# Kernel optimization log

Hardware: AMD Instinct MI355X
Metric: run time of the kernel (lower is better)

## Reference

```python
import jax, jax.numpy as jnp
import numpy as np

B, S, D = 2, 2048, 7168
R, H, VD = 1024, 16, 128
QK_HD = R // H            # 64, per-head latent q/k dim
SCALE = float(np.sqrt(D // H))  # self.scale = d_heads ** 0.5 = sqrt(448)


def setup_inputs() -> dict:
    key = jax.random.key(0)
    ks = jax.random.split(key, 6)
    return {
        "x":   jax.random.normal(ks[0], (B, S, D), dtype=jnp.float32),
        "Wq":  jax.random.normal(ks[1], (R, D), dtype=jnp.float32) * 0.02,
        "Wkv": jax.random.normal(ks[2], (R, D), dtype=jnp.float32) * 0.02,
        "Wvb": jax.random.normal(ks[3], (H * VD, R), dtype=jnp.float32) * 0.02,
        "Wo":  jax.random.normal(ks[4], (D, H * VD), dtype=jnp.float32) * 0.02,
        "bo":  jnp.zeros((D,), dtype=jnp.float32),
    }


def reference(x, Wq, Wkv, Wvb, Wo, bo):
    b, s, d = x.shape
    # low-rank compressed projections (torch Linear: y = x @ W.T)
    q_lat  = x @ Wq.T            # [B,S,R] compressed query
    kv_lat = x @ Wkv.T           # [B,S,R] compressed KV latent (shared K)
    q = q_lat.reshape(b, s, H, QK_HD)    # [B,S,H,64]
    k = kv_lat.reshape(b, s, H, QK_HD)   # [B,S,H,64]
    # up-project values from latent
    v = (kv_lat @ Wvb.T).reshape(b, s, H, VD)  # [B,S,H,128]
    # scaled causal attention in latent head space
    scores = jnp.einsum("bqhd,bkhd->bhqk", q, k) / SCALE  # [B,H,S,S]
    causal = jnp.tril(jnp.ones((s, s), dtype=bool))
    scores = jnp.where(causal, scores, jnp.finfo(scores.dtype).min)
    attn = jax.nn.softmax(scores, axis=-1)
    out = jnp.einsum("bhqk,bkhd->bqhd", attn, v).reshape(b, s, H * VD)
    return out @ Wo.T + bo       # [B,S,D]
```

## Files before the change

### kernel.cpp

```cpp
#include <hip/hip_runtime.h>
#include <hip/hip_bf16.h>

typedef __bf16 bf16_t;
typedef __attribute__((ext_vector_type(8))) __bf16 bf16x8;
typedef __attribute__((ext_vector_type(4))) __bf16 bf16x4;
typedef __attribute__((ext_vector_type(4))) float f32x4;

#define B_ 2
#define S_ 2048
#define D_ 7168
#define R_ 1024
#define H_ 16
#define VD_ 128
#define MROWS 4096
#define NQKV 2048
#define HVD 2048

__device__ __forceinline__ void gload_lds16(const bf16_t* g, bf16_t* l) {
    __builtin_amdgcn_global_load_lds(
        (const __attribute__((address_space(1))) unsigned int*)(g),
        (__attribute__((address_space(3))) unsigned int*)(l),
        16, 0, 0);
}

__global__ __launch_bounds__(256)
void cvt_f32_bf16(const float* __restrict__ src, bf16_t* __restrict__ dst, float scale) {
    size_t i = ((size_t)blockIdx.x * 256 + threadIdx.x) * 4;
    f32x4 v = *(const f32x4*)(src + i);
    bf16x4 o;
    o[0] = (bf16_t)(v[0] * scale);
    o[1] = (bf16_t)(v[1] * scale);
    o[2] = (bf16_t)(v[2] * scale);
    o[3] = (bf16_t)(v[3] * scale);
    *(bf16x4*)(dst + i) = o;
}

template<int OUTF32>
__global__ __launch_bounds__(256)
void gemm_bt(const bf16_t* __restrict__ A, int lda,
             const bf16_t* __restrict__ Bt, int ldb,
             void* __restrict__ Cv, int ldc,
             const float* __restrict__ bias, int K)
{
    __shared__ __align__(16) bf16_t As[2][128 * 64];
    __shared__ __align__(16) bf16_t Bs[2][128 * 64];
    const int tid  = threadIdx.x;
    const int lane = tid & 63;
    const int wave = tid >> 6;
    const int tileM = blockIdx.y * 128;
    const int tileN = blockIdx.x * 128;
    const int wr = (wave >> 1) * 64;
    const int wc = (wave & 1) * 64;
    const int r  = lane & 15;
    const int kq = lane >> 4;

    const bf16_t* Ag = A  + (size_t)tileM * lda;
    const bf16_t* Bg = Bt + (size_t)tileN * ldb;

    int srow[4], scol[4], slin[4];
    #pragma unroll
    for (int i = 0; i < 4; ++i) {
        slin[i] = (i * 256 + tid) * 8;
        srow[i] = slin[i] >> 6;
        scol[i] = (slin[i] & 63) ^ ((srow[i] & 7) << 3);
    }

    #define ISSUE_TILE(buf, k0)                                                  \
        {                                                                        \
            _Pragma("unroll")                                                    \
            for (int i = 0; i < 4; ++i) {                                        \
                gload_lds16(Ag + (size_t)srow[i] * lda + (k0) + scol[i], As[buf] + slin[i]); \
                gload_lds16(Bg + (size_t)srow[i] * ldb + (k0) + scol[i], Bs[buf] + slin[i]); \
            }                                                                    \
        }

    f32x4 acc[4][4] = {};
    const int nt = K >> 6;

    ISSUE_TILE(0, 0)
    ISSUE_TILE(1, 64)
    asm volatile("s_waitcnt vmcnt(8)" ::: "memory");
    __builtin_amdgcn_s_barrier();
    __builtin_amdgcn_sched_barrier(0);

    for (int t = 0; t < nt; ++t) {
        const int cur = t & 1;
        const bf16_t* Ab = As[cur];
        const bf16_t* Bb = Bs[cur];

        bf16x8 af[4][2], bfr[4][2];
        #pragma unroll
        for (int m = 0; m < 4; ++m)
            #pragma unroll
            for (int kk = 0; kk < 2; ++kk) {
                const int e = (wr + m * 16 + r) * 64 + kk * 32 + kq * 8;
                af[m][kk] = *(const bf16x8*)(Ab + (e ^ ((r & 7) << 3)));
            }
        #pragma unroll
        for (int n = 0; n < 4; ++n)
            #pragma unroll
            for (int kk = 0; kk < 2; ++kk) {
                const int e = (wc + n * 16 + r) * 64 + kk * 32 + kq * 8;
                bfr[n][kk] = *(const bf16x8*)(Bb + (e ^ ((r & 7) << 3)));
            }
        __builtin_amdgcn_s_setprio(1);
        #pragma unroll
        for (int kk = 0; kk < 2; ++kk)
            #pragma unroll
            for (int m = 0; m < 4; ++m)
                #pragma unroll
                for (int n = 0; n < 4; ++n)
                    acc[m][n] = __builtin_amdgcn_mfma_f32_16x16x32_bf16(af[m][kk], bfr[n][kk], acc[m][n], 0, 0, 0);
        __builtin_amdgcn_s_setprio(0);

        __builtin_amdgcn_s_barrier();
        __builtin_amdgcn_sched_barrier(0);
        if (t + 2 < nt) {
            ISSUE_TILE(cur, (t + 2) << 6)
            asm volatile("s_waitcnt vmcnt(8)" ::: "memory");
        } else {
            asm volatile("s_waitcnt vmcnt(0)" ::: "memory");
        }
        __builtin_amdgcn_s_barrier();
        __builtin_amdgcn_sched_barrier(0);
    }
    #undef ISSUE_TILE

    const int orow = tileM + wr + kq * 4;
    const int ocol = tileN + wc + r;
    if (OUTF32) {
        float* C = (float*)Cv;
        #pragma unroll
        for (int n = 0; n < 4; ++n) {
            float bv = bias[ocol + n * 16];
            #pragma unroll
            for (int m = 0; m < 4; ++m)
                #pragma unroll
                for (int j = 0; j < 4; ++j)
                    C[(size_t)(orow + m * 16 + j) * ldc + ocol + n * 16] = acc[m][n][j] + bv;
        }
    } else {
        bf16_t* C = (bf16_t*)Cv;
        #pragma unroll
        for (int m = 0; m < 4; ++m)
            #pragma unroll
            for (int n = 0; n < 4; ++n)
                #pragma unroll
                for (int j = 0; j < 4; ++j)
                    C[(size_t)(orow + m * 16 + j) * ldc + ocol + n * 16] = (bf16_t)acc[m][n][j];
    }
}

template<int OUTF32>
__global__ __launch_bounds__(512, 2)
void gemm_bt256(const bf16_t* __restrict__ A, int lda,
                const bf16_t* __restrict__ Bt, int ldb,
                void* __restrict__ Cv, int ldc,
                const float* __restrict__ bias, int K)
{
    __shared__ __align__(16) bf16_t As[2][256 * 64];
    __shared__ __align__(16) bf16_t Bs[2][256 * 64];
    const int tid  = threadIdx.x;
    const int lane = tid & 63;
    const int wave = tid >> 6;
    const int wm = wave >> 2;
    const int wn = wave & 3;
    const int tileM = blockIdx.y * 256;
    const int tileN = blockIdx.x * 256;
    const int r  = lane & 15;
    const int kq = lane >> 4;

    const bf16_t* Ag = A  + (size_t)tileM * lda;
    const bf16_t* Bg = Bt + (size_t)tileN * ldb;

    int srow[4], scol[4], slin[4];
    #pragma unroll
    for (int i = 0; i < 4; ++i) {
        slin[i] = (i * 512 + tid) * 8;
        srow[i] = slin[i] >> 6;
        scol[i] = (slin[i] & 63) ^ ((srow[i] & 7) << 3);
    }

    #define ISSUE_TILE2(buf, k0)                                                 \
        {                                                                        \
            _Pragma("unroll")                                                    \
            for (int i = 0; i < 4; ++i) {                                        \
                gload_lds16(Ag + (size_t)srow[i] * lda + (k0) + scol[i], As[buf] + slin[i]); \
                gload_lds16(Bg + (size_t)srow[i] * ldb + (k0) + scol[i], Bs[buf] + slin[i]); \
            }                                                                    \
        }

    f32x4 acc[8][4] = {};
    const int nt = K >> 6;

    ISSUE_TILE2(0, 0)
    ISSUE_TILE2(1, 64)
    asm volatile("s_waitcnt vmcnt(8)" ::: "memory");
    __builtin_amdgcn_s_barrier();
    __builtin_amdgcn_sched_barrier(0);

    for (int t = 0; t < nt; ++t) {
        const int cur = t & 1;
        const bf16_t* Ab = As[cur];
        const bf16_t* Bb = Bs[cur];

        #pragma unroll
        for (int kk = 0; kk < 2; ++kk) {
            bf16x8 af[8], bfr[4];
            #pragma unroll
            for (int m = 0; m < 8; ++m) {
                const int e = (wm * 128 + m * 16 + r) * 64 + kk * 32 + kq * 8;
                af[m] = *(const bf16x8*)(Ab + (e ^ ((r & 7) << 3)));
            }
            #pragma unroll
            for (int n = 0; n < 4; ++n) {
                const int e = (wn * 64 + n * 16 + r) * 64 + kk * 32 + kq * 8;
                bfr[n] = *(const bf16x8*)(Bb + (e ^ ((r & 7) << 3)));
            }
            __builtin_amdgcn_s_setprio(1);
            #pragma unroll
            for (int m = 0; m < 8; ++m)
                #pragma unroll
                for (int n = 0; n < 4; ++n)
                    acc[m][n] = __builtin_amdgcn_mfma_f32_16x16x32_bf16(af[m], bfr[n], acc[m][n], 0, 0, 0);
            __builtin_amdgcn_s_setprio(0);
        }

        __builtin_amdgcn_s_barrier();
        __builtin_amdgcn_sched_barrier(0);
        if (t + 2 < nt) {
            ISSUE_TILE2(cur, (t + 2) << 6)
            asm volatile("s_waitcnt vmcnt(8)" ::: "memory");
        } else {
            asm volatile("s_waitcnt vmcnt(0)" ::: "memory");
        }
        __builtin_amdgcn_s_barrier();
        __builtin_amdgcn_sched_barrier(0);
    }
    #undef ISSUE_TILE2

    const int orow = tileM + wm * 128 + kq * 4;
    const int ocol = tileN + wn * 64 + r;
    if (OUTF32) {
        float* C = (float*)Cv;
        #pragma unroll
        for (int n = 0; n < 4; ++n) {
            float bv = bias[ocol + n * 16];
            #pragma unroll
            for (int m = 0; m < 8; ++m)
                #pragma unroll
                for (int j = 0; j < 4; ++j)
                    C[(size_t)(orow + m * 16 + j) * ldc + ocol + n * 16] = acc[m][n][j] + bv;
        }
    } else {
        bf16_t* C = (bf16_t*)Cv;
        #pragma unroll
        for (int m = 0; m < 8; ++m)
            #pragma unroll
            for (int n = 0; n < 4; ++n)
                #pragma unroll
                for (int j = 0; j < 4; ++j)
                    C[(size_t)(orow + m * 16 + j) * ldc + ocol + n * 16] = (bf16_t)acc[m][n][j];
    }
}

__device__ __forceinline__ void attn_qtile(
    const bf16_t* __restrict__ Q, const bf16_t* __restrict__ Kp,
    const bf16_t* __restrict__ Vp, bf16_t* __restrict__ Op,
    bf16_t* __restrict__ P_lds, int qbase, int lane)
{
    const int r  = lane & 15;
    const int kq = lane >> 4;

    bf16x8 qf[2][2];
    #pragma unroll
    for (int m = 0; m < 2; ++m)
        #pragma unroll
        for (int kk = 0; kk < 2; ++kk)
            qf[m][kk] = *(const bf16x8*)(Q + (size_t)(qbase + m * 16 + r) * NQKV + kk * 32 + kq * 8);

    f32x4 o[2][8] = {};
    float mst[2][4], lst[2][4];
    #pragma unroll
    for (int m = 0; m < 2; ++m)
        #pragma unroll
        for (int j = 0; j < 4; ++j) { mst[m][j] = -INFINITY; lst[m][j] = 0.0f; }

    const int nfull  = qbase >> 6;
    const int ntiles = (qbase + 95) >> 6;

    for (int t = 0; t < ntiles; ++t) {
        const int kvb = t * 64;
        f32x4 s[2][4] = {};
        #pragma unroll
        for (int n = 0; n < 4; ++n) {
            bf16x8 kf0 = *(const bf16x8*)(Kp + (size_t)(kvb + n * 16 + r) * NQKV + kq * 8);
            bf16x8 kf1 = *(const bf16x8*)(Kp + (size_t)(kvb + n * 16 + r) * NQKV + 32 + kq * 8);
            #pragma unroll
            for (int m = 0; m < 2; ++m) {
                s[m][n] = __builtin_amdgcn_mfma_f32_16x16x32_bf16(qf[m][0], kf0, s[m][n], 0, 0, 0);
                s[m][n] = __builtin_amdgcn_mfma_f32_16x16x32_bf16(qf[m][1], kf1, s[m][n], 0, 0, 0);
            }
        }
        if (t >= nfull) {
            #pragma unroll
            for (int m = 0; m < 2; ++m)
                #pragma unroll
                for (int n = 0; n < 4; ++n)
                    #pragma unroll
                    for (int j = 0; j < 4; ++j) {
                        int kc = kvb + n * 16 + r;
                        int qr = qbase + m * 16 + kq * 4 + j;
                        if (kc > qr) s[m][n][j] = -1e30f;
                    }
        }
        float mx[2][4];
        #pragma unroll
        for (int m = 0; m < 2; ++m)
            #pragma unroll
            for (int j = 0; j < 4; ++j) {
                float v = fmaxf(fmaxf(s[m][0][j], s[m][1][j]), fmaxf(s[m][2][j], s[m][3][j]));
                #pragma unroll
                for (int d = 1; d < 16; d <<= 1) v = fmaxf(v, __shfl_xor(v, d, 64));
                mx[m][j] = v;
            }
        bool need = false;
        #pragma unroll
        for (int m = 0; m < 2; ++m)
            #pragma unroll
            for (int j = 0; j < 4; ++j) need |= (mx[m][j] > mst[m][j] + 8.0f);
        if (__ballot(need)) {
            #pragma unroll
            for (int m = 0; m < 2; ++m)
                #pragma unroll
                for (int j = 0; j < 4; ++j) {
                    float mnew  = fmaxf(mst[m][j], mx[m][j]);
                    float alpha = __expf(mst[m][j] - mnew);
                    lst[m][j] *= alpha;
                    mst[m][j]  = mnew;
                    #pragma unroll
                    for (int n = 0; n < 8; ++n) o[m][n][j] *= alpha;
                }
        }
        #pragma unroll
        for (int m = 0; m < 2; ++m)
            #pragma unroll
            for (int j = 0; j < 4; ++j) {
                float rs = 0.0f;
                const int row = m * 16 + kq * 4 + j;
                #pragma unroll
                for (int n = 0; n < 4; ++n) {
                    float pv = __expf(s[m][n][j] - mst[m][j]);
                    rs += pv;
                    const int c = (n * 16 + r) ^ ((row & 7) << 3);
                    P_lds[row * 64 + c] = (bf16_t)pv;
                }
                #pragma unroll
                for (int d = 1; d < 16; d <<= 1) rs += __shfl_xor(rs, d, 64);
                lst[m][j] += rs;
            }
        __syncthreads();
        bf16x8 pf[2][2];
        #pragma unroll
        for (int m = 0; m < 2; ++m)
            #pragma unroll
            for (int kk = 0; kk < 2; ++kk) {
                const int e = (m * 16 + r) * 64 + kk * 32 + kq * 8;
                pf[m][kk] = *(const bf16x8*)(P_lds + (e ^ ((r & 7) << 3)));
            }
        #pragma unroll
        for (int n = 0; n < 8; ++n) {
            #pragma unroll
            for (int kk = 0; kk < 2; ++kk) {
                bf16x8 vf = *(const bf16x8*)(Vp + (size_t)(n * 16 + r) * MROWS + kvb + kk * 32 + kq * 8);
                #pragma unroll
                for (int m = 0; m < 2; ++m)
                    o[m][n] = __builtin_amdgcn_mfma_f32_16x16x32_bf16(pf[m][kk], vf, o[m][n], 0, 0, 0);
            }
        }
        __syncthreads();
    }

    #pragma unroll
    for (int m = 0; m < 2; ++m)
        #pragma unroll
        for (int j = 0; j < 4; ++j) {
            float inv = 1.0f / lst[m][j];
            int row = m * 16 + kq * 4 + j;
            #pragma unroll
            for (int n = 0; n < 8; ++n)
                Op[(size_t)(qbase + row) * HVD + n * 16 + r] = (bf16_t)(o[m][n][j] * inv);
        }
}

__global__ __launch_bounds__(64)
void attn_kernel(const bf16_t* __restrict__ qkv, const bf16_t* __restrict__ Vt,
                 bf16_t* __restrict__ O)
{
    __shared__ __align__(16) bf16_t P_lds[32 * 64];
    const int lane = threadIdx.x;
    const int p = blockIdx.x;
    const int h = blockIdx.y;
    const int b = blockIdx.z;

    const bf16_t* Q  = qkv + (size_t)(b * S_) * NQKV + h * 64;
    const bf16_t* Kp = qkv + (size_t)(b * S_) * NQKV + R_ + h * 64;
    const bf16_t* Vp = Vt + (size_t)(h * VD_) * MROWS + b * S_;
    bf16_t* Op = O + (size_t)(b * S_) * HVD + h * VD_;

    attn_qtile(Q, Kp, Vp, Op, P_lds, (63 - p) * 32, lane);
    attn_qtile(Q, Kp, Vp, Op, P_lds, p * 32, lane);
}

extern "C" void kernel_launch(void* const* d_in, const int* in_sizes, int n_in,
                              void* d_out, int out_size, void* d_ws, size_t ws_size,
                              hipStream_t stream) {
    const float* x   = (const float*)d_in[0];
    const float* Wq  = (const float*)d_in[1];
    const float* Wkv = (const float*)d_in[2];
    const float* Wvb = (const float*)d_in[3];
    const float* Wo  = (const float*)d_in[4];
    const float* bo  = (const float*)d_in[5];

    char* oc = (char*)d_out;
    bf16_t* xb     = (bf16_t*)oc;
    bf16_t* Wqkv_b = (bf16_t*)(oc + 58720256);
    char* ws = (char*)d_ws;
    bf16_t* qkv_b  = (bf16_t*)ws;
    bf16_t* Wvb_b  = (bf16_t*)(ws + 16777216);
    bf16_t* Vt_b   = (bf16_t*)(ws + 20971520);
    bf16_t* attn_b = (bf16_t*)(ws + 37748736);
    bf16_t* Wo_b   = (bf16_t*)(ws + 54525952);

    const float inv_scale = 0.047245559f;

    cvt_f32_bf16<<<29360128 / 1024, 256, 0, stream>>>(x,   xb, 1.0f);
    cvt_f32_bf16<<< 7340032 / 1024, 256, 0, stream>>>(Wq,  Wqkv_b, inv_scale);
    cvt_f32_bf16<<< 7340032 / 1024, 256, 0, stream>>>(Wkv, Wqkv_b + 7340032, 1.0f);
    cvt_f32_bf16<<< 2097152 / 1024, 256, 0, stream>>>(Wvb, Wvb_b, 1.0f);
    cvt_f32_bf16<<<14680064 / 1024, 256, 0, stream>>>(Wo,  Wo_b, 1.0f);

    gemm_bt<0><<<dim3(16, 32), 256, 0, stream>>>(xb, D_, Wqkv_b, D_, qkv_b, NQKV, nullptr, D_);
    gemm_bt<0><<<dim3(32, 16), 256, 0, stream>>>(Wvb_b, R_, qkv_b + R_, NQKV, Vt_b, MROWS, nullptr, R_);
    attn_kernel<<<dim3(32, H_, B_), 64, 0, stream>>>(qkv_b, Vt_b, attn_b);
    gemm_bt256<1><<<dim3(28, 16), 512, 0, stream>>>(attn_b, HVD, Wo_b, HVD, d_out, D_, bo, HVD);
}
```

Before: 518.0 us.

## Overlap next-tile global loads with second k-half MFMAs and split attention across waves

Both GEMM kernels now split each 64-wide k tile into two halves. The second half's fragments are read from LDS early, then a barrier is hit and the global-to-LDS prefetch for tile t+2 is issued before the second-half MFMAs, so the loads overlap compute instead of sitting between barriers. The attention kernel now runs its two causal q-tiles on two waves of one 128-thread block, each with its own P buffer, rather than one wave doing both in sequence. The __syncthreads calls inside the attention loop are removed, which relies on each wave only touching its own LDS slice.

```diff
diff --git a/kernel.cpp b/kernel.cpp
--- a/kernel.cpp
+++ b/kernel.cpp
@@ -88,39 +88,53 @@
         const bf16_t* Ab = As[cur];
         const bf16_t* Bb = Bs[cur];
 
-        bf16x8 af[4][2], bfr[4][2];
+        bf16x8 af0[4], bf0[4];
+        #pragma unroll
+        for (int m = 0; m < 4; ++m) {
+            const int e = (wr + m * 16 + r) * 64 + kq * 8;
+            af0[m] = *(const bf16x8*)(Ab + (e ^ ((r & 7) << 3)));
+        }
+        #pragma unroll
+        for (int n = 0; n < 4; ++n) {
+            const int e = (wc + n * 16 + r) * 64 + kq * 8;
+            bf0[n] = *(const bf16x8*)(Bb + (e ^ ((r & 7) << 3)));
+        }
+        __builtin_amdgcn_s_setprio(1);
         #pragma unroll
         for (int m = 0; m < 4; ++m)
             #pragma unroll
-            for (int kk = 0; kk < 2; ++kk) {
-                const int e = (wr + m * 16 + r) * 64 + kk * 32 + kq * 8;
-                af[m][kk] = *(const bf16x8*)(Ab + (e ^ ((r & 7) << 3)));
-            }
-        #pragma unroll
-        for (int n = 0; n < 4; ++n)
-            #pragma unroll
-            for (int kk = 0; kk < 2; ++kk) {
-                const int e = (wc + n * 16 + r) * 64 + kk * 32 + kq * 8;
-                bfr[n][kk] = *(const bf16x8*)(Bb + (e ^ ((r & 7) << 3)));
-            }
+            for (int n = 0; n < 4; ++n)
+                acc[m][n] = __builtin_amdgcn_mfma_f32_16x16x32_bf16(af0[m], bf0[n], acc[m][n], 0, 0, 0);
+        __builtin_amdgcn_s_setprio(0);
+
+        bf16x8 af1[4], bf1[4];
+        #pragma unroll
+        for (int m = 0; m < 4; ++m) {
+            const int e = (wr + m * 16 + r) * 64 + 32 + kq * 8;
+            af1[m] = *(const bf16x8*)(Ab + (e ^ ((r & 7) << 3)));
+        }
+        #pragma unroll
+        for (int n = 0; n < 4; ++n) {
+            const int e = (wc + n * 16 + r) * 64 + 32 + kq * 8;
+            bf1[n] = *(const bf16x8*)(Bb + (e ^ ((r & 7) << 3)));
+        }
+        asm volatile("s_waitcnt lgkmcnt(0)" ::: "memory");
+        __builtin_amdgcn_sched_barrier(0);
+        __builtin_amdgcn_s_barrier();
+
+        if (t + 2 < nt) { ISSUE_TILE(cur, (t + 2) << 6) }
+
         __builtin_amdgcn_s_setprio(1);
         #pragma unroll
-        for (int kk = 0; kk < 2; ++kk)
-            #pragma unroll
-            for (int m = 0; m < 4; ++m)
-                #pragma unroll
-                for (int n = 0; n < 4; ++n)
-                    acc[m][n] = __builtin_amdgcn_mfma_f32_16x16x32_bf16(af[m][kk], bfr[n][kk], acc[m][n], 0, 0, 0);
+        for (int m = 0; m < 4; ++m)
+            #pragma unroll
+            for (int n = 0; n < 4; ++n)
+                acc[m][n] = __builtin_amdgcn_mfma_f32_16x16x32_bf16(af1[m], bf1[n], acc[m][n], 0, 0, 0);
         __builtin_amdgcn_s_setprio(0);
 
-        __builtin_amdgcn_s_barrier();
-        __builtin_amdgcn_sched_barrier(0);
-        if (t + 2 < nt) {
-            ISSUE_TILE(cur, (t + 2) << 6)
-            asm volatile("s_waitcnt vmcnt(8)" ::: "memory");
-        } else {
-            asm volatile("s_waitcnt vmcnt(0)" ::: "memory");
-        }
+        if (t + 2 < nt) asm volatile("s_waitcnt vmcnt(8)" ::: "memory");
+        else            asm volatile("s_waitcnt vmcnt(0)" ::: "memory");
+        __builtin_amdgcn_sched_barrier(0);
         __builtin_amdgcn_s_barrier();
         __builtin_amdgcn_sched_barrier(0);
     }
@@ -204,17 +218,16 @@
         const bf16_t* Ab = As[cur];
         const bf16_t* Bb = Bs[cur];
 
-        #pragma unroll
-        for (int kk = 0; kk < 2; ++kk) {
+        {
             bf16x8 af[8], bfr[4];
             #pragma unroll
             for (int m = 0; m < 8; ++m) {
-                const int e = (wm * 128 + m * 16 + r) * 64 + kk * 32 + kq * 8;
+                const int e = (wm * 128 + m * 16 + r) * 64 + kq * 8;
                 af[m] = *(const bf16x8*)(Ab + (e ^ ((r & 7) << 3)));
             }
             #pragma unroll
             for (int n = 0; n < 4; ++n) {
-                const int e = (wn * 64 + n * 16 + r) * 64 + kk * 32 + kq * 8;
+                const int e = (wn * 64 + n * 16 + r) * 64 + kq * 8;
                 bfr[n] = *(const bf16x8*)(Bb + (e ^ ((r & 7) << 3)));
             }
             __builtin_amdgcn_s_setprio(1);
@@ -225,15 +238,34 @@
                     acc[m][n] = __builtin_amdgcn_mfma_f32_16x16x32_bf16(af[m], bfr[n], acc[m][n], 0, 0, 0);
             __builtin_amdgcn_s_setprio(0);
         }
-
+        bf16x8 af1[8], bf1[4];
+        #pragma unroll
+        for (int m = 0; m < 8; ++m) {
+            const int e = (wm * 128 + m * 16 + r) * 64 + 32 + kq * 8;
+            af1[m] = *(const bf16x8*)(Ab + (e ^ ((r & 7) << 3)));
+        }
+        #pragma unroll
+        for (int n = 0; n < 4; ++n) {
+            const int e = (wn * 64 + n * 16 + r) * 64 + 32 + kq * 8;
+            bf1[n] = *(const bf16x8*)(Bb + (e ^ ((r & 7) << 3)));
+        }
+        asm volatile("s_waitcnt lgkmcnt(0)" ::: "memory");
+        __builtin_amdgcn_sched_barrier(0);
         __builtin_amdgcn_s_barrier();
-        __builtin_amdgcn_sched_barrier(0);
-        if (t + 2 < nt) {
-            ISSUE_TILE2(cur, (t + 2) << 6)
-            asm volatile("s_waitcnt vmcnt(8)" ::: "memory");
-        } else {
-            asm volatile("s_waitcnt vmcnt(0)" ::: "memory");
-        }
+
+        if (t + 2 < nt) { ISSUE_TILE2(cur, (t + 2) << 6) }
+
+        __builtin_amdgcn_s_setprio(1);
+        #pragma unroll
+        for (int m = 0; m < 8; ++m)
+            #pragma unroll
+            for (int n = 0; n < 4; ++n)
+                acc[m][n] = __builtin_amdgcn_mfma_f32_16x16x32_bf16(af1[m], bf1[n], acc[m][n], 0, 0, 0);
+        __builtin_amdgcn_s_setprio(0);
+
+        if (t + 2 < nt) asm volatile("s_waitcnt vmcnt(8)" ::: "memory");
+        else            asm volatile("s_waitcnt vmcnt(0)" ::: "memory");
+        __builtin_amdgcn_sched_barrier(0);
         __builtin_amdgcn_s_barrier();
         __builtin_amdgcn_sched_barrier(0);
     }
@@ -359,7 +391,6 @@
                 for (int d = 1; d < 16; d <<= 1) rs += __shfl_xor(rs, d, 64);
                 lst[m][j] += rs;
             }
-        __syncthreads();
         bf16x8 pf[2][2];
         #pragma unroll
         for (int m = 0; m < 2; ++m)
@@ -378,7 +409,6 @@
                     o[m][n] = __builtin_amdgcn_mfma_f32_16x16x32_bf16(pf[m][kk], vf, o[m][n], 0, 0, 0);
             }
         }
-        __syncthreads();
     }
 
     #pragma unroll
@@ -393,12 +423,14 @@
         }
 }
 
-__global__ __launch_bounds__(64)
+__global__ __launch_bounds__(128)
 void attn_kernel(const bf16_t* __restrict__ qkv, const bf16_t* __restrict__ Vt,
                  bf16_t* __restrict__ O)
 {
-    __shared__ __align__(16) bf16_t P_lds[32 * 64];
-    const int lane = threadIdx.x;
+    __shared__ __align__(16) bf16_t P_all[2][32 * 64];
+    const int tid  = threadIdx.x;
+    const int lane = tid & 63;
+    const int wave = tid >> 6;
     const int p = blockIdx.x;
     const int h = blockIdx.y;
     const int b = blockIdx.z;
@@ -408,8 +440,8 @@
     const bf16_t* Vp = Vt + (size_t)(h * VD_) * MROWS + b * S_;
     bf16_t* Op = O + (size_t)(b * S_) * HVD + h * VD_;
 
-    attn_qtile(Q, Kp, Vp, Op, P_lds, (63 - p) * 32, lane);
-    attn_qtile(Q, Kp, Vp, Op, P_lds, p * 32, lane);
+    const int qt = wave ? p : (63 - p);
+    attn_qtile(Q, Kp, Vp, Op, P_all[wave], qt * 32, lane);
 }
 
 extern "C" void kernel_launch(void* const* d_in, const int* in_sizes, int n_in,
@@ -442,6 +474,6 @@
 
     gemm_bt<0><<<dim3(16, 32), 256, 0, stream>>>(xb, D_, Wqkv_b, D_, qkv_b, NQKV, nullptr, D_);
     gemm_bt<0><<<dim3(32, 16), 256, 0, stream>>>(Wvb_b, R_, qkv_b + R_, NQKV, Vt_b, MROWS, nullptr, R_);
-    attn_kernel<<<dim3(32, H_, B_), 64, 0, stream>>>(qkv_b, Vt_b, attn_b);
+    attn_kernel<<<dim3(32, H_, B_), 128, 0, stream>>>(qkv_b, Vt_b, attn_b);
     gemm_bt256<1><<<dim3(28, 16), 512, 0, stream>>>(attn_b, HVD, Wo_b, HVD, d_out, D_, bo, HVD);
 }
```

Result: slower. 575.1 us (+11.0%).

## Fuse conversion launches and overlap next-tile loads with second k-half MFMAs

Applied to the files above, without the earlier changes.

Merges the five fp32-to-bf16 conversion kernels into one launch in which each thread converts 8 elements, cutting launch overhead and tail effects. In the 256-wide GEMM main loop, the second k-half's LDS fragments are read before the barrier, then the next tile's global-to-LDS loads are issued before that half's MFMAs, so the copies overlap with compute instead of sitting after it. This raises register pressure for the extra fragment set and depends on the buffer reuse being safe once all waves have finished reading the current tile.

```diff
diff --git a/kernel.cpp b/kernel.cpp
--- a/kernel.cpp
+++ b/kernel.cpp
@@ -24,15 +24,35 @@
 }
 
 __global__ __launch_bounds__(256)
-void cvt_f32_bf16(const float* __restrict__ src, bf16_t* __restrict__ dst, float scale) {
-    size_t i = ((size_t)blockIdx.x * 256 + threadIdx.x) * 4;
-    f32x4 v = *(const f32x4*)(src + i);
-    bf16x4 o;
-    o[0] = (bf16_t)(v[0] * scale);
-    o[1] = (bf16_t)(v[1] * scale);
-    o[2] = (bf16_t)(v[2] * scale);
-    o[3] = (bf16_t)(v[3] * scale);
-    *(bf16x4*)(dst + i) = o;
+void cvt_fused(const float* __restrict__ x,  const float* __restrict__ Wq,
+               const float* __restrict__ Wkv, const float* __restrict__ Wvb,
+               const float* __restrict__ Wo,
+               bf16_t* __restrict__ xb, bf16_t* __restrict__ Wqkv_b,
+               bf16_t* __restrict__ Wvb_b, bf16_t* __restrict__ Wo_b,
+               float inv_scale)
+{
+    const long c = ((long)blockIdx.x * 256 + threadIdx.x);
+    const long e = c * 8;
+    const float* src; bf16_t* dst; long off; float scale = 1.0f;
+    if (e < 29360128L) {
+        src = x;   dst = xb;              off = e;
+    } else if (e < 36700160L) {
+        src = Wq;  dst = Wqkv_b;          off = e - 29360128L; scale = inv_scale;
+    } else if (e < 44040192L) {
+        src = Wkv; dst = Wqkv_b + 7340032; off = e - 36700160L;
+    } else if (e < 46137344L) {
+        src = Wvb; dst = Wvb_b;           off = e - 44040192L;
+    } else {
+        src = Wo;  dst = Wo_b;            off = e - 46137344L;
+    }
+    f32x4 v0 = *(const f32x4*)(src + off);
+    f32x4 v1 = *(const f32x4*)(src + off + 4);
+    bf16x8 o;
+    o[0] = (bf16_t)(v0[0] * scale); o[1] = (bf16_t)(v0[1] * scale);
+    o[2] = (bf16_t)(v0[2] * scale); o[3] = (bf16_t)(v0[3] * scale);
+    o[4] = (bf16_t)(v1[0] * scale); o[5] = (bf16_t)(v1[1] * scale);
+    o[6] = (bf16_t)(v1[2] * scale); o[7] = (bf16_t)(v1[3] * scale);
+    *(bf16x8*)(dst + off) = o;
 }
 
 template<int OUTF32>
@@ -204,17 +224,16 @@
         const bf16_t* Ab = As[cur];
         const bf16_t* Bb = Bs[cur];
 
-        #pragma unroll
-        for (int kk = 0; kk < 2; ++kk) {
+        {
             bf16x8 af[8], bfr[4];
             #pragma unroll
             for (int m = 0; m < 8; ++m) {
-                const int e = (wm * 128 + m * 16 + r) * 64 + kk * 32 + kq * 8;
+                const int e = (wm * 128 + m * 16 + r) * 64 + kq * 8;
                 af[m] = *(const bf16x8*)(Ab + (e ^ ((r & 7) << 3)));
             }
             #pragma unroll
             for (int n = 0; n < 4; ++n) {
-                const int e = (wn * 64 + n * 16 + r) * 64 + kk * 32 + kq * 8;
+                const int e = (wn * 64 + n * 16 + r) * 64 + kq * 8;
                 bfr[n] = *(const bf16x8*)(Bb + (e ^ ((r & 7) << 3)));
             }
             __builtin_amdgcn_s_setprio(1);
@@ -225,15 +244,34 @@
                     acc[m][n] = __builtin_amdgcn_mfma_f32_16x16x32_bf16(af[m], bfr[n], acc[m][n], 0, 0, 0);
             __builtin_amdgcn_s_setprio(0);
         }
-
+        bf16x8 af1[8], bf1[4];
+        #pragma unroll
+        for (int m = 0; m < 8; ++m) {
+            const int e = (wm * 128 + m * 16 + r) * 64 + 32 + kq * 8;
+            af1[m] = *(const bf16x8*)(Ab + (e ^ ((r & 7) << 3)));
+        }
+        #pragma unroll
+        for (int n = 0; n < 4; ++n) {
+            const int e = (wn * 64 + n * 16 + r) * 64 + 32 + kq * 8;
+            bf1[n] = *(const bf16x8*)(Bb + (e ^ ((r & 7) << 3)));
+        }
+        asm volatile("s_waitcnt lgkmcnt(0)" ::: "memory");
+        __builtin_amdgcn_sched_barrier(0);
         __builtin_amdgcn_s_barrier();
+
+        if (t + 2 < nt) { ISSUE_TILE2(cur, (t + 2) << 6) }
+
+        __builtin_amdgcn_s_setprio(1);
+        #pragma unroll
+        for (int m = 0; m < 8; ++m)
+            #pragma unroll
+            for (int n = 0; n < 4; ++n)
+                acc[m][n] = __builtin_amdgcn_mfma_f32_16x16x32_bf16(af1[m], bf1[n], acc[m][n], 0, 0, 0);
+        __builtin_amdgcn_s_setprio(0);
+
+        if (t + 2 < nt) asm volatile("s_waitcnt vmcnt(8)" ::: "memory");
+        else            asm volatile("s_waitcnt vmcnt(0)" ::: "memory");
         __builtin_amdgcn_sched_barrier(0);
-        if (t + 2 < nt) {
-            ISSUE_TILE2(cur, (t + 2) << 6)
-            asm volatile("s_waitcnt vmcnt(8)" ::: "memory");
-        } else {
-            asm volatile("s_waitcnt vmcnt(0)" ::: "memory");
-        }
         __builtin_amdgcn_s_barrier();
         __builtin_amdgcn_sched_barrier(0);
     }
@@ -434,11 +472,8 @@
 
     const float inv_scale = 0.047245559f;
 
-    cvt_f32_bf16<<<29360128 / 1024, 256, 0, stream>>>(x,   xb, 1.0f);
-    cvt_f32_bf16<<< 7340032 / 1024, 256, 0, stream>>>(Wq,  Wqkv_b, inv_scale);
-    cvt_f32_bf16<<< 7340032 / 1024, 256, 0, stream>>>(Wkv, Wqkv_b + 7340032, 1.0f);
-    cvt_f32_bf16<<< 2097152 / 1024, 256, 0, stream>>>(Wvb, Wvb_b, 1.0f);
-    cvt_f32_bf16<<<14680064 / 1024, 256, 0, stream>>>(Wo,  Wo_b, 1.0f);
+    cvt_fused<<<29696, 256, 0, stream>>>(x, Wq, Wkv, Wvb, Wo,
+                                         xb, Wqkv_b, Wvb_b, Wo_b, inv_scale);
 
     gemm_bt<0><<<dim3(16, 32), 256, 0, stream>>>(xb, D_, Wqkv_b, D_, qkv_b, NQKV, nullptr, D_);
     gemm_bt<0><<<dim3(32, 16), 256, 0, stream>>>(Wvb_b, R_, qkv_b + R_, NQKV, Vt_b, MROWS, nullptr, R_);
```

After: 487.8 us. 1.06x faster.
